# Performance work log

Measured on AMD Instinct MI355X. Metric: run time of the kernel, lower is better.

The kernel has to match this reference:

```python
import jax, jax.numpy as jnp
import numpy as np

D_MODEL = 1024
N_HEADS = 16
HEAD_DIM = D_MODEL // N_HEADS  # 64
WINDOW = 64
HALF = WINDOW // 2  # query i attends keys in [i-HALF, i+HALF]
CHUNK = WINDOW      # chunk size for banded attention; must be >= HALF and divide S
B, S = 4, 4096


def setup_inputs() -> dict:
    key = jax.random.key(0)
    ks = jax.random.split(key, 6)
    s = 0.02
    D = D_MODEL
    return {
        "x":  jax.random.normal(ks[0], (B, S, D), jnp.float32),
        "Wq": jax.random.normal(ks[1], (D, D), jnp.float32) * s,
        "bq": jnp.zeros((D,), jnp.float32),
        "Wk": jax.random.normal(ks[2], (D, D), jnp.float32) * s,
        "bk": jnp.zeros((D,), jnp.float32),
        "Wv": jax.random.normal(ks[3], (D, D), jnp.float32) * s,
        "bv": jnp.zeros((D,), jnp.float32),
        "Wo": jax.random.normal(ks[4], (D, D), jnp.float32) * s,
        "bo": jnp.zeros((D,), jnp.float32),
    }


def reference(x, Wq, bq, Wk, bk, Wv, bv, Wo, bo):
    # Sliding-window attention (seq_len > 128 path of SparseAttention).
    b, s, d = x.shape
    h, hd = N_HEADS, HEAD_DIM
    scale = 1.0 / np.sqrt(hd).astype(np.float32)

    q = (x @ Wq.T + bq).reshape(b, s, h, hd)
    k = (x @ Wk.T + bk).reshape(b, s, h, hd)
    v = (x @ Wv.T + bv).reshape(b, s, h, hd)

    c = CHUNK
    nb = s // c
    qc = q.reshape(b, nb, c, h, hd)

    # Pad one chunk of zeros on each side; each query chunk attends keys in
    # chunks [n-1, n, n+1] (covers the +/-HALF band since HALF <= c).
    pad = jnp.zeros((b, c, h, hd), q.dtype)
    kp = jnp.concatenate([pad, k, pad], axis=1).reshape(b, nb + 2, c, h, hd)
    vp = jnp.concatenate([pad, v, pad], axis=1).reshape(b, nb + 2, c, h, hd)
    k3 = jnp.concatenate([kp[:, :-2], kp[:, 1:-1], kp[:, 2:]], axis=2)  # [b,nb,3c,h,hd]
    v3 = jnp.concatenate([vp[:, :-2], vp[:, 1:-1], vp[:, 2:]], axis=2)

    # scores: [b,h,nb,c,3c]
    scores = jnp.einsum('bnqhd,bnkhd->bhnqk', qc, k3) * scale

    # Banded validity mask. Global query pos = n*c + i ; global key pos = n*c + j - c.
    i = jnp.arange(c)[:, None]          # [c,1]
    j = jnp.arange(3 * c)[None, :]      # [1,3c]
    rel = j - c - i                     # key_pos - query_pos, [c,3c]
    band = (rel >= -HALF) & (rel <= HALF)
    n = jnp.arange(nb)[:, None, None]   # [nb,1,1]
    keypos = n * c + (j - c)[None, :, :]  # [nb,1,3c]
    valid = band[None, :, :] & (keypos >= 0) & (keypos < s)  # [nb,c,3c]

    attn = jax.nn.softmax(jnp.where(valid[None, None], scores, -jnp.inf), axis=-1)
    ctx = jnp.einsum('bhnqk,bnkhd->bnqhd', attn, v3).reshape(b, s, d)
    return ctx @ Wo.T + bo
```

## Files before the change

kernel.cpp:

```cpp
#include <hip/hip_runtime.h>
#include <hip/hip_bf16.h>
#include <cstdint>
#include <cstddef>

#define D_MODEL 1024
#define NHEADS  16
#define HDIM    64
#define HALFW   32
#define BATCH   4
#define SEQ     4096
#define MROWS   (BATCH*SEQ)

typedef __attribute__((ext_vector_type(8))) short        bf16x8;
typedef __attribute__((ext_vector_type(4))) float        f32x4;
typedef __attribute__((ext_vector_type(4))) unsigned int u32x4;

typedef const __attribute__((address_space(1))) void gvoid_t;
typedef __attribute__((address_space(3))) void       lvoid_t;

__device__ __forceinline__ unsigned short f2bf(float f) {
    unsigned int u = __float_as_uint(f);
    u += 0x7fffu + ((u >> 16) & 1u);
    return (unsigned short)(u >> 16);
}

__device__ __forceinline__ int vswz(int row, int bytecol) {
    return (row * 256 + bytecol) ^ (((row ^ (row >> 3)) & 7) << 4);
}

__global__ __launch_bounds__(256)
void cvt_f32_bf16(const float* __restrict__ src, unsigned short* __restrict__ dst, int n8) {
    int i = blockIdx.x * 256 + threadIdx.x;
    if (i >= n8) return;
    float4 a = *(const float4*)(src + (size_t)i * 8);
    float4 b = *(const float4*)(src + (size_t)i * 8 + 4);
    u32x4 o;
    o[0] = (unsigned)f2bf(a.x) | ((unsigned)f2bf(a.y) << 16);
    o[1] = (unsigned)f2bf(a.z) | ((unsigned)f2bf(a.w) << 16);
    o[2] = (unsigned)f2bf(b.x) | ((unsigned)f2bf(b.y) << 16);
    o[3] = (unsigned)f2bf(b.z) | ((unsigned)f2bf(b.w) << 16);
    *(u32x4*)(dst + (size_t)i * 8) = o;
}

__global__ __launch_bounds__(256)
void cvt4_f32_bf16(const float* __restrict__ s0, const float* __restrict__ s1,
                   const float* __restrict__ s2, const float* __restrict__ s3,
                   unsigned short* __restrict__ d0, unsigned short* __restrict__ d1,
                   unsigned short* __restrict__ d2, unsigned short* __restrict__ d3, int n8) {
    int i = blockIdx.x * 256 + threadIdx.x;
    if (i >= n8) return;
    const float* src = blockIdx.y == 0 ? s0 : blockIdx.y == 1 ? s1 : blockIdx.y == 2 ? s2 : s3;
    unsigned short* dst = blockIdx.y == 0 ? d0 : blockIdx.y == 1 ? d1 : blockIdx.y == 2 ? d2 : d3;
    float4 a = *(const float4*)(src + (size_t)i * 8);
    float4 b = *(const float4*)(src + (size_t)i * 8 + 4);
    u32x4 o;
    o[0] = (unsigned)f2bf(a.x) | ((unsigned)f2bf(a.y) << 16);
    o[1] = (unsigned)f2bf(a.z) | ((unsigned)f2bf(a.w) << 16);
    o[2] = (unsigned)f2bf(b.x) | ((unsigned)f2bf(b.y) << 16);
    o[3] = (unsigned)f2bf(b.z) | ((unsigned)f2bf(b.w) << 16);
    *(u32x4*)(dst + (size_t)i * 8) = o;
}

template <int NOUT, int F32OUT>
__global__ __launch_bounds__(256, 2)
void gemm_db(const unsigned short* __restrict__ A,
             const unsigned short* __restrict__ W0,
             const unsigned short* __restrict__ W1,
             const unsigned short* __restrict__ W2,
             const float* __restrict__ b0, const float* __restrict__ b1,
             const float* __restrict__ b2,
             unsigned short* __restrict__ o0, unsigned short* __restrict__ o1,
             unsigned short* __restrict__ o2, float* __restrict__ of32)
{
    constexpr int K  = 1024;
    constexpr int HT = K / 32;
    constexpr int CBG = 8 * NOUT;
    __shared__ unsigned short lds[2 * 12288];

    const int tid  = threadIdx.x;
    const int wave = tid >> 6, lane = tid & 63;
    const int wr = wave >> 1, wc = wave & 1;

    const int bid = blockIdx.x;
    const int g   = (bid & 7) * (8 * CBG) + (bid >> 3);
    const int rb  = g / CBG;
    const int cbg = g % CBG;
    const int which = cbg >> 3;
    const int bm = rb * 256, bn = (cbg & 7) * 128;

    const unsigned short* W = (NOUT == 1 || which == 0) ? W0 : (which == 1 ? W1 : W2);
    const float* bias       = (NOUT == 1 || which == 0) ? b0 : (which == 1 ? b1 : b2);
    unsigned short* obf     = (NOUT == 1 || which == 0) ? o0 : (which == 1 ? o1 : o2);

    f32x4 acc[8][4];
    #pragma unroll
    for (int m = 0; m < 8; ++m)
        #pragma unroll
        for (int n = 0; n < 4; ++n)
            #pragma unroll
            for (int j = 0; j < 4; ++j) acc[m][n][j] = 0.0f;

    char* ldsb = (char*)lds;

    const int ra  = tid >> 2;
    const int ks  = ((tid & 3) - (ra >> 1)) & 3;
    const size_t sA[4] = { (size_t)(bm + ra) * K + ks * 8,
                           (size_t)(bm + ra + 64)  * K + ks * 8,
                           (size_t)(bm + ra + 128) * K + ks * 8,
                           (size_t)(bm + ra + 192) * K + ks * 8 };
    const size_t sB[2] = { (size_t)(bn + ra) * K + ks * 8,
                           (size_t)(bn + ra + 64)  * K + ks * 8 };
    const int ldsW = wave * 1024;

    auto STAGE = [&](int h) {
        const int slot = (h & 1) * 24576;
        const int ke = h * 32;
        #pragma unroll
        for (int i = 0; i < 4; ++i)
            __builtin_amdgcn_global_load_lds((gvoid_t*)(A + sA[i] + ke),
                (lvoid_t*)(ldsb + slot + ldsW + i * 4096), 16, 0, 0);
        #pragma unroll
        for (int i = 0; i < 2; ++i)
            __builtin_amdgcn_global_load_lds((gvoid_t*)(W + sB[i] + ke),
                (lvoid_t*)(ldsb + slot + 16384 + ldsW + i * 4096), 16, 0, 0);
    };

    const int lr = lane & 15;
    const int pp = (((lane >> 4) + (lr >> 1)) & 3) << 4;
    const int abase = (wr * 128 + lr) * 64 + pp;
    const int bbase = 16384 + (wc * 64 + lr) * 64 + pp;

    STAGE(0);
    __syncthreads();

    #pragma unroll 1
    for (int h = 0; h < HT; ++h) {
        const char* sl = ldsb + (h & 1) * 24576;
        if (h + 1 < HT) STAGE(h + 1);
        bf16x8 fa[8], fb[4];
        #pragma unroll
        for (int m = 0; m < 8; ++m) fa[m] = *(const bf16x8*)(sl + abase + m * 1024);
        #pragma unroll
        for (int n = 0; n < 4; ++n) fb[n] = *(const bf16x8*)(sl + bbase + n * 1024);
        #pragma unroll
        for (int m = 0; m < 8; ++m)
            #pragma unroll
            for (int n = 0; n < 4; ++n)
                acc[m][n] = __builtin_amdgcn_mfma_f32_16x16x32_bf16(fa[m], fb[n], acc[m][n], 0, 0, 0);
        __syncthreads();
    }

    float bvv[4];
    #pragma unroll
    for (int n = 0; n < 4; ++n) bvv[n] = bias[bn + wc * 64 + n * 16 + lr];
    #pragma unroll
    for (int m = 0; m < 8; ++m) {
        #pragma unroll
        for (int j = 0; j < 4; ++j) {
            const int row = bm + wr * 128 + m * 16 + (lane >> 4) * 4 + j;
            #pragma unroll
            for (int n = 0; n < 4; ++n) {
                const int col = bn + wc * 64 + n * 16 + lr;
                const float v = acc[m][n][j] + bvv[n];
                if (F32OUT) of32[(size_t)row * 1024 + col] = v;
                else        obf[(size_t)row * 1024 + col]  = f2bf(v);
            }
        }
    }
}

__global__ __launch_bounds__(256)
void attn_band(const unsigned short* __restrict__ Q,
               const unsigned short* __restrict__ Kk,
               const unsigned short* __restrict__ V,
               unsigned short* __restrict__ Ctx)
{
    __shared__ unsigned short Qs[64 * 72];
    __shared__ unsigned short Ks[128 * 72];
    __shared__ unsigned short Vt[64 * 128];
    __shared__ unsigned short Ps[64 * 128];

    const int qt = blockIdx.x, h = blockIdx.y, b = blockIdx.z;
    const int qbase  = qt * 64;
    const int kstart = qbase - HALFW;
    const int tid = threadIdx.x, wave = tid >> 6, lane = tid & 63;

    const size_t base = (size_t)b * SEQ * D_MODEL + (size_t)h * HDIM;
    const unsigned short* Qb = Q  + base;
    const unsigned short* Kb = Kk + base;
    const unsigned short* Vb = V  + base;
    unsigned short*       Cb = Ctx + base;

    for (int c = tid; c < 512; c += 256) {
        const int row = c >> 3, col = (c & 7) * 8;
        *(u32x4*)(Qs + row * 72 + col) =
            *(const u32x4*)(Qb + (size_t)(qbase + row) * D_MODEL + col);
    }
    for (int c = tid; c < 1024; c += 256) {
        const int krow = c >> 3, col = (c & 7) * 8;
        const int kpos = kstart + krow;
        u32x4 kv;
        if (kpos >= 0 && kpos < SEQ) {
            kv = *(const u32x4*)(Kb + (size_t)kpos * D_MODEL + col);
        } else {
            for (int j = 0; j < 4; ++j) kv[j] = 0u;
        }
        *(u32x4*)(Ks + krow * 72 + col) = kv;
    }
    for (int c = tid; c < 512; c += 256) {
        const int p = c >> 3, dch = c & 7;
        const int k0 = kstart + 2 * p, k1 = k0 + 1;
        u32x4 v0, v1;
        if (k0 >= 0 && k0 < SEQ) {
            v0 = *(const u32x4*)(Vb + (size_t)k0 * D_MODEL + dch * 8);
        } else {
            for (int j = 0; j < 4; ++j) v0[j] = 0u;
        }
        if (k1 >= 0 && k1 < SEQ) {
            v1 = *(const u32x4*)(Vb + (size_t)k1 * D_MODEL + dch * 8);
        } else {
            for (int j = 0; j < 4; ++j) v1[j] = 0u;
        }
        #pragma unroll
        for (int j = 0; j < 8; ++j) {
            const int d = dch * 8 + j;
            const unsigned lo = (v0[j >> 1] >> ((j & 1) * 16)) & 0xffffu;
            const unsigned hi = (v1[j >> 1] >> ((j & 1) * 16)) & 0xffffu;
            *(unsigned*)((char*)Vt + vswz(d, 4 * p)) = lo | (hi << 16);
        }
    }
    __syncthreads();

    f32x4 sc[8];
    #pragma unroll
    for (int c = 0; c < 8; ++c)
        #pragma unroll
        for (int j = 0; j < 4; ++j) sc[c][j] = 0.0f;

    bf16x8 aq[2];
    #pragma unroll
    for (int kc = 0; kc < 2; ++kc)
        aq[kc] = *(const bf16x8*)(Qs + (wave * 16 + (lane & 15)) * 72 + kc * 32 + (lane >> 4) * 8);
    #pragma unroll
    for (int c = 0; c < 8; ++c) {
        #pragma unroll
        for (int kc = 0; kc < 2; ++kc) {
            bf16x8 bk_ = *(const bf16x8*)(Ks + (c * 16 + (lane & 15)) * 72 + kc * 32 + (lane >> 4) * 8);
            sc[c] = __builtin_amdgcn_mfma_f32_16x16x32_bf16(aq[kc], bk_, sc[c], 0, 0, 0);
        }
    }

    const int grp = lane >> 4, colk = lane & 15;
    float rowmax[4] = {-1e30f, -1e30f, -1e30f, -1e30f};
    #pragma unroll
    for (int c = 0; c < 8; ++c) {
        const int kpos = kstart + c * 16 + colk;
        #pragma unroll
        for (int j = 0; j < 4; ++j) {
            const int qpos = qbase + wave * 16 + grp * 4 + j;
            const int rel = kpos - qpos;
            const bool valid = (kpos >= 0) && (kpos < SEQ) && (rel >= -HALFW) && (rel <= HALFW);
            const float v = valid ? sc[c][j] * 0.125f : -1e30f;
            sc[c][j] = v;
            rowmax[j] = fmaxf(rowmax[j], v);
        }
    }
    #pragma unroll
    for (int j = 0; j < 4; ++j)
        #pragma unroll
        for (int m = 1; m < 16; m <<= 1)
            rowmax[j] = fmaxf(rowmax[j], __shfl_xor(rowmax[j], m, 64));

    float rowsum[4] = {0.f, 0.f, 0.f, 0.f};
    #pragma unroll
    for (int c = 0; c < 8; ++c)
        #pragma unroll
        for (int j = 0; j < 4; ++j) {
            const float p = __expf(sc[c][j] - rowmax[j]);
            sc[c][j] = p;
            rowsum[j] += p;
        }
    #pragma unroll
    for (int j = 0; j < 4; ++j)
        #pragma unroll
        for (int m = 1; m < 16; m <<= 1)
            rowsum[j] += __shfl_xor(rowsum[j], m, 64);

    #pragma unroll
    for (int c = 0; c < 8; ++c)
        #pragma unroll
        for (int j = 0; j < 4; ++j)
            *(unsigned short*)((char*)Ps + vswz(wave * 16 + grp * 4 + j, (c * 16 + colk) * 2))
                = f2bf(sc[c][j]);
    __syncthreads();

    f32x4 o[4];
    #pragma unroll
    for (int n = 0; n < 4; ++n)
        #pragma unroll
        for (int j = 0; j < 4; ++j) o[n][j] = 0.0f;
    #pragma unroll
    for (int kc = 0; kc < 4; ++kc) {
        bf16x8 pa = *(const bf16x8*)((const char*)Ps +
                        vswz(wave * 16 + (lane & 15), kc * 64 + (lane >> 4) * 16));
        #pragma unroll
        for (int n = 0; n < 4; ++n) {
            bf16x8 bv_ = *(const bf16x8*)((const char*)Vt +
                            vswz(n * 16 + (lane & 15), kc * 64 + (lane >> 4) * 16));
            o[n] = __builtin_amdgcn_mfma_f32_16x16x32_bf16(pa, bv_, o[n], 0, 0, 0);
        }
    }

    float rinv[4];
    #pragma unroll
    for (int j = 0; j < 4; ++j) rinv[j] = 1.0f / rowsum[j];
    #pragma unroll
    for (int n = 0; n < 4; ++n)
        #pragma unroll
        for (int j = 0; j < 4; ++j) {
            const int q = qbase + wave * 16 + grp * 4 + j;
            Cb[(size_t)q * D_MODEL + n * 16 + colk] = f2bf(o[n][j] * rinv[j]);
        }
}

extern "C" void kernel_launch(void* const* d_in, const int* in_sizes, int n_in,
                              void* d_out, int out_size, void* d_ws, size_t ws_size,
                              hipStream_t stream)
{
    (void)in_sizes; (void)n_in; (void)out_size; (void)ws_size;
    const float* x  = (const float*)d_in[0];
    const float* Wq = (const float*)d_in[1];
    const float* bq = (const float*)d_in[2];
    const float* Wk = (const float*)d_in[3];
    const float* bk = (const float*)d_in[4];
    const float* Wv = (const float*)d_in[5];
    const float* bv = (const float*)d_in[6];
    const float* Wo = (const float*)d_in[7];
    const float* bo = (const float*)d_in[8];
    float* out = (float*)d_out;

    char* ws = (char*)d_ws;
    unsigned short* xb  = (unsigned short*)ws;
    unsigned short* wqb = (unsigned short*)(ws + 33554432);
    unsigned short* wkb = wqb + 1048576;
    unsigned short* wvb = wkb + 1048576;
    unsigned short* wob = wvb + 1048576;
    unsigned short* qb  = wob + 1048576;
    unsigned short* kb  = qb + (size_t)MROWS * D_MODEL;
    unsigned short* vb  = kb + (size_t)MROWS * D_MODEL;
    unsigned short* ctxb = xb;

    cvt_f32_bf16<<<dim3(MROWS * D_MODEL / 8 / 256), 256, 0, stream>>>(x, xb, MROWS * D_MODEL / 8);
    cvt4_f32_bf16<<<dim3(D_MODEL * D_MODEL / 8 / 256, 4), 256, 0, stream>>>(
        Wq, Wk, Wv, Wo, wqb, wkb, wvb, wob, D_MODEL * D_MODEL / 8);

    gemm_db<3, 0><<<dim3(1536), 256, 0, stream>>>(
        xb, wqb, wkb, wvb, bq, bk, bv, qb, kb, vb, nullptr);

    attn_band<<<dim3(SEQ / 64, NHEADS, BATCH), 256, 0, stream>>>(qb, kb, vb, ctxb);

    gemm_db<1, 1><<<dim3(512), 256, 0, stream>>>(
        ctxb, wob, wob, wob, bo, bo, bo, nullptr, nullptr, nullptr, out);
}
```

Baseline: 232.5 us.

## Fuse fp32-to-bf16 input conversion into QKV GEMM and read Q/K directly in attention

Removes the separate x conversion kernel. The QKV GEMM now loads fp32 x into registers, packs it to bf16 with v_cvt_pk_bf16_f32 and writes it into LDS itself, overlapped with the MFMA loop. This avoids a full write and re-read of the bf16 copy of x. The attention kernel drops its Q/K LDS staging and one barrier, loading MFMA fragments straight from global memory. In exchange the GEMM reads twice as many bytes of A per tile, needs more registers, and the attention K loads can go out of the sequence range; those reads land in adjacent workspace and their scores are masked.

```diff
diff --git a/kernel.cpp b/kernel.cpp
--- a/kernel.cpp
+++ b/kernel.cpp
@@ -24,22 +24,14 @@
     return (unsigned short)(u >> 16);
 }
 
+__device__ __forceinline__ unsigned cvtpk(float lo, float hi) {
+    unsigned r;
+    asm("v_cvt_pk_bf16_f32 %0, %1, %2" : "=v"(r) : "v"(lo), "v"(hi));
+    return r;
+}
+
 __device__ __forceinline__ int vswz(int row, int bytecol) {
     return (row * 256 + bytecol) ^ (((row ^ (row >> 3)) & 7) << 4);
-}
-
-__global__ __launch_bounds__(256)
-void cvt_f32_bf16(const float* __restrict__ src, unsigned short* __restrict__ dst, int n8) {
-    int i = blockIdx.x * 256 + threadIdx.x;
-    if (i >= n8) return;
-    float4 a = *(const float4*)(src + (size_t)i * 8);
-    float4 b = *(const float4*)(src + (size_t)i * 8 + 4);
-    u32x4 o;
-    o[0] = (unsigned)f2bf(a.x) | ((unsigned)f2bf(a.y) << 16);
-    o[1] = (unsigned)f2bf(a.z) | ((unsigned)f2bf(a.w) << 16);
-    o[2] = (unsigned)f2bf(b.x) | ((unsigned)f2bf(b.y) << 16);
-    o[3] = (unsigned)f2bf(b.z) | ((unsigned)f2bf(b.w) << 16);
-    *(u32x4*)(dst + (size_t)i * 8) = o;
 }
 
 __global__ __launch_bounds__(256)
@@ -61,20 +53,19 @@
     *(u32x4*)(dst + (size_t)i * 8) = o;
 }
 
-template <int NOUT, int F32OUT>
 __global__ __launch_bounds__(256, 2)
-void gemm_db(const unsigned short* __restrict__ A,
-             const unsigned short* __restrict__ W0,
-             const unsigned short* __restrict__ W1,
-             const unsigned short* __restrict__ W2,
-             const float* __restrict__ b0, const float* __restrict__ b1,
-             const float* __restrict__ b2,
-             unsigned short* __restrict__ o0, unsigned short* __restrict__ o1,
-             unsigned short* __restrict__ o2, float* __restrict__ of32)
+void gemm_qkv(const float* __restrict__ X,
+              const unsigned short* __restrict__ W0,
+              const unsigned short* __restrict__ W1,
+              const unsigned short* __restrict__ W2,
+              const float* __restrict__ b0, const float* __restrict__ b1,
+              const float* __restrict__ b2,
+              unsigned short* __restrict__ o0, unsigned short* __restrict__ o1,
+              unsigned short* __restrict__ o2)
 {
     constexpr int K  = 1024;
     constexpr int HT = K / 32;
-    constexpr int CBG = 8 * NOUT;
+    constexpr int CBG = 24;
     __shared__ unsigned short lds[2 * 12288];
 
     const int tid  = threadIdx.x;
@@ -88,9 +79,126 @@
     const int which = cbg >> 3;
     const int bm = rb * 256, bn = (cbg & 7) * 128;
 
-    const unsigned short* W = (NOUT == 1 || which == 0) ? W0 : (which == 1 ? W1 : W2);
-    const float* bias       = (NOUT == 1 || which == 0) ? b0 : (which == 1 ? b1 : b2);
-    unsigned short* obf     = (NOUT == 1 || which == 0) ? o0 : (which == 1 ? o1 : o2);
+    const unsigned short* W = which == 0 ? W0 : (which == 1 ? W1 : W2);
+    const float* bias       = which == 0 ? b0 : (which == 1 ? b1 : b2);
+    unsigned short* obf     = which == 0 ? o0 : (which == 1 ? o1 : o2);
+
+    f32x4 acc[8][4];
+    #pragma unroll
+    for (int m = 0; m < 8; ++m)
+        #pragma unroll
+        for (int n = 0; n < 4; ++n)
+            #pragma unroll
+            for (int j = 0; j < 4; ++j) acc[m][n][j] = 0.0f;
+
+    char* ldsb = (char*)lds;
+
+    const int ra   = tid >> 2;
+    const int posk = tid & 3;
+    const int ks   = (posk - (ra >> 1)) & 3;
+    size_t sAf[4];
+    #pragma unroll
+    for (int i = 0; i < 4; ++i) sAf[i] = (size_t)(bm + ra + 64 * i) * K + ks * 8;
+    const size_t sB[2] = { (size_t)(bn + ra) * K + ks * 8,
+                           (size_t)(bn + ra + 64) * K + ks * 8 };
+    const int ldsW = wave * 1024;
+    const int aWrite = ra * 64 + posk * 16;
+
+    float4 av[8];
+
+    auto LOADA = [&](int h) {
+        const int ke = h * 32;
+        #pragma unroll
+        for (int i = 0; i < 4; ++i) {
+            av[2 * i]     = *(const float4*)(X + sAf[i] + ke);
+            av[2 * i + 1] = *(const float4*)(X + sAf[i] + ke + 4);
+        }
+    };
+    auto STAGE_B = [&](int h) {
+        const int slot = (h & 1) * 24576;
+        const int ke = h * 32;
+        #pragma unroll
+        for (int i = 0; i < 2; ++i)
+            __builtin_amdgcn_global_load_lds((gvoid_t*)(W + sB[i] + ke),
+                (lvoid_t*)(ldsb + slot + 16384 + ldsW + i * 4096), 16, 0, 0);
+    };
+    auto CVTWR = [&](int h) {
+        const int slot = (h & 1) * 24576;
+        #pragma unroll
+        for (int i = 0; i < 4; ++i) {
+            u32x4 o;
+            o[0] = cvtpk(av[2 * i].x,     av[2 * i].y);
+            o[1] = cvtpk(av[2 * i].z,     av[2 * i].w);
+            o[2] = cvtpk(av[2 * i + 1].x, av[2 * i + 1].y);
+            o[3] = cvtpk(av[2 * i + 1].z, av[2 * i + 1].w);
+            *(u32x4*)(ldsb + slot + i * 4096 + aWrite) = o;
+        }
+    };
+
+    const int lr = lane & 15;
+    const int pp = (((lane >> 4) + (lr >> 1)) & 3) << 4;
+    const int abase = (wr * 128 + lr) * 64 + pp;
+    const int bbase = 16384 + (wc * 64 + lr) * 64 + pp;
+
+    LOADA(0); STAGE_B(0); CVTWR(0);
+    __syncthreads();
+
+    #pragma unroll 1
+    for (int h = 0; h < HT; ++h) {
+        const char* sl = ldsb + (h & 1) * 24576;
+        if (h + 1 < HT) { LOADA(h + 1); STAGE_B(h + 1); }
+        bf16x8 fa[8], fb[4];
+        #pragma unroll
+        for (int m = 0; m < 8; ++m) fa[m] = *(const bf16x8*)(sl + abase + m * 1024);
+        #pragma unroll
+        for (int n = 0; n < 4; ++n) fb[n] = *(const bf16x8*)(sl + bbase + n * 1024);
+        #pragma unroll
+        for (int m = 0; m < 8; ++m)
+            #pragma unroll
+            for (int n = 0; n < 4; ++n)
+                acc[m][n] = __builtin_amdgcn_mfma_f32_16x16x32_bf16(fa[m], fb[n], acc[m][n], 0, 0, 0);
+        if (h + 1 < HT) CVTWR(h + 1);
+        __syncthreads();
+    }
+
+    float bvv[4];
+    #pragma unroll
+    for (int n = 0; n < 4; ++n) bvv[n] = bias[bn + wc * 64 + n * 16 + lr];
+    #pragma unroll
+    for (int m = 0; m < 8; ++m) {
+        #pragma unroll
+        for (int j = 0; j < 4; ++j) {
+            const int row = bm + wr * 128 + m * 16 + (lane >> 4) * 4 + j;
+            #pragma unroll
+            for (int n = 0; n < 4; ++n) {
+                const int col = bn + wc * 64 + n * 16 + lr;
+                obf[(size_t)row * 1024 + col] = f2bf(acc[m][n][j] + bvv[n]);
+            }
+        }
+    }
+}
+
+template <int NOUT, int F32OUT>
+__global__ __launch_bounds__(256, 2)
+void gemm_db(const unsigned short* __restrict__ A,
+             const unsigned short* __restrict__ W0,
+             const float* __restrict__ b0,
+             unsigned short* __restrict__ o0, float* __restrict__ of32)
+{
+    constexpr int K  = 1024;
+    constexpr int HT = K / 32;
+    constexpr int CBG = 8 * NOUT;
+    __shared__ unsigned short lds[2 * 12288];
+
+    const int tid  = threadIdx.x;
+    const int wave = tid >> 6, lane = tid & 63;
+    const int wr = wave >> 1, wc = wave & 1;
+
+    const int bid = blockIdx.x;
+    const int g   = (bid & 7) * (8 * CBG) + (bid >> 3);
+    const int rb  = g / CBG;
+    const int cbg = g % CBG;
+    const int bm = rb * 256, bn = (cbg & 7) * 128;
 
     f32x4 acc[8][4];
     #pragma unroll
@@ -121,7 +229,7 @@
                 (lvoid_t*)(ldsb + slot + ldsW + i * 4096), 16, 0, 0);
         #pragma unroll
         for (int i = 0; i < 2; ++i)
-            __builtin_amdgcn_global_load_lds((gvoid_t*)(W + sB[i] + ke),
+            __builtin_amdgcn_global_load_lds((gvoid_t*)(W0 + sB[i] + ke),
                 (lvoid_t*)(ldsb + slot + 16384 + ldsW + i * 4096), 16, 0, 0);
     };
 
@@ -152,7 +260,7 @@
 
     float bvv[4];
     #pragma unroll
-    for (int n = 0; n < 4; ++n) bvv[n] = bias[bn + wc * 64 + n * 16 + lr];
+    for (int n = 0; n < 4; ++n) bvv[n] = b0[bn + wc * 64 + n * 16 + lr];
     #pragma unroll
     for (int m = 0; m < 8; ++m) {
         #pragma unroll
@@ -163,7 +271,7 @@
                 const int col = bn + wc * 64 + n * 16 + lr;
                 const float v = acc[m][n][j] + bvv[n];
                 if (F32OUT) of32[(size_t)row * 1024 + col] = v;
-                else        obf[(size_t)row * 1024 + col]  = f2bf(v);
+                else        o0[(size_t)row * 1024 + col]  = f2bf(v);
             }
         }
     }
@@ -175,8 +283,6 @@
                const unsigned short* __restrict__ V,
                unsigned short* __restrict__ Ctx)
 {
-    __shared__ unsigned short Qs[64 * 72];
-    __shared__ unsigned short Ks[128 * 72];
     __shared__ unsigned short Vt[64 * 128];
     __shared__ unsigned short Ps[64 * 128];
 
@@ -191,22 +297,6 @@
     const unsigned short* Vb = V  + base;
     unsigned short*       Cb = Ctx + base;
 
-    for (int c = tid; c < 512; c += 256) {
-        const int row = c >> 3, col = (c & 7) * 8;
-        *(u32x4*)(Qs + row * 72 + col) =
-            *(const u32x4*)(Qb + (size_t)(qbase + row) * D_MODEL + col);
-    }
-    for (int c = tid; c < 1024; c += 256) {
-        const int krow = c >> 3, col = (c & 7) * 8;
-        const int kpos = kstart + krow;
-        u32x4 kv;
-        if (kpos >= 0 && kpos < SEQ) {
-            kv = *(const u32x4*)(Kb + (size_t)kpos * D_MODEL + col);
-        } else {
-            for (int j = 0; j < 4; ++j) kv[j] = 0u;
-        }
-        *(u32x4*)(Ks + krow * 72 + col) = kv;
-    }
     for (int c = tid; c < 512; c += 256) {
         const int p = c >> 3, dch = c & 7;
         const int k0 = kstart + 2 * p, k1 = k0 + 1;
@@ -237,15 +327,19 @@
         #pragma unroll
         for (int j = 0; j < 4; ++j) sc[c][j] = 0.0f;
 
+    const int fcol = (lane >> 4) * 8;
     bf16x8 aq[2];
     #pragma unroll
     for (int kc = 0; kc < 2; ++kc)
-        aq[kc] = *(const bf16x8*)(Qs + (wave * 16 + (lane & 15)) * 72 + kc * 32 + (lane >> 4) * 8);
+        aq[kc] = *(const bf16x8*)(Qb + (size_t)(qbase + wave * 16 + (lane & 15)) * D_MODEL
+                                     + kc * 32 + fcol);
     #pragma unroll
     for (int c = 0; c < 8; ++c) {
+        const long krow = (long)kstart + c * 16 + (lane & 15);
+        const unsigned short* kp = Kb + krow * (long)D_MODEL + fcol;
         #pragma unroll
         for (int kc = 0; kc < 2; ++kc) {
-            bf16x8 bk_ = *(const bf16x8*)(Ks + (c * 16 + (lane & 15)) * 72 + kc * 32 + (lane >> 4) * 8);
+            bf16x8 bk_ = *(const bf16x8*)(kp + kc * 32);
             sc[c] = __builtin_amdgcn_mfma_f32_16x16x32_bf16(aq[kc], bk_, sc[c], 0, 0, 0);
         }
     }
@@ -292,7 +386,6 @@
         for (int j = 0; j < 4; ++j)
             *(unsigned short*)((char*)Ps + vswz(wave * 16 + grp * 4 + j, (c * 16 + colk) * 2))
                 = f2bf(sc[c][j]);
-    __syncthreads();
 
     f32x4 o[4];
     #pragma unroll
@@ -340,7 +433,7 @@
     float* out = (float*)d_out;
 
     char* ws = (char*)d_ws;
-    unsigned short* xb  = (unsigned short*)ws;
+    unsigned short* ctxb = (unsigned short*)ws;
     unsigned short* wqb = (unsigned short*)(ws + 33554432);
     unsigned short* wkb = wqb + 1048576;
     unsigned short* wvb = wkb + 1048576;
@@ -348,17 +441,15 @@
     unsigned short* qb  = wob + 1048576;
     unsigned short* kb  = qb + (size_t)MROWS * D_MODEL;
     unsigned short* vb  = kb + (size_t)MROWS * D_MODEL;
-    unsigned short* ctxb = xb;
-
-    cvt_f32_bf16<<<dim3(MROWS * D_MODEL / 8 / 256), 256, 0, stream>>>(x, xb, MROWS * D_MODEL / 8);
+
     cvt4_f32_bf16<<<dim3(D_MODEL * D_MODEL / 8 / 256, 4), 256, 0, stream>>>(
         Wq, Wk, Wv, Wo, wqb, wkb, wvb, wob, D_MODEL * D_MODEL / 8);
 
-    gemm_db<3, 0><<<dim3(1536), 256, 0, stream>>>(
-        xb, wqb, wkb, wvb, bq, bk, bv, qb, kb, vb, nullptr);
+    gemm_qkv<<<dim3(1536), 256, 0, stream>>>(
+        x, wqb, wkb, wvb, bq, bk, bv, qb, kb, vb);
 
     attn_band<<<dim3(SEQ / 64, NHEADS, BATCH), 256, 0, stream>>>(qb, kb, vb, ctxb);
 
     gemm_db<1, 1><<<dim3(512), 256, 0, stream>>>(
-        ctxb, wob, wob, wob, bo, bo, bo, nullptr, nullptr, nullptr, out);
-}
+        ctxb, wob, bo, nullptr, out);
+}
```

New measurement: 267.6 us. 1.15x slower.

## Load GEMM weights and attention Q/K straight from global into registers

Applied to the files above, without the earlier changes.

The projection GEMM no longer stages the weight tile in LDS. Each wave loads its B fragments directly from global memory into registers every K-step, which halves the LDS footprint, and the block-to-tile mapping is reordered. The attention kernel drops its Q and K shared-memory staging and reads the MFMA fragments straight from global; the barrier before the P·V stage is removed because each wave reads only its own P rows. The aim is less LDS traffic and fewer barriers, at the cost of exposed global-load latency with no prefetch, and out-of-range K reads at the sequence edges that are then masked.

```diff
diff --git a/kernel.cpp b/kernel.cpp
--- a/kernel.cpp
+++ b/kernel.cpp
@@ -63,7 +63,7 @@
 
 template <int NOUT, int F32OUT>
 __global__ __launch_bounds__(256, 2)
-void gemm_db(const unsigned short* __restrict__ A,
+void gemm_bd(const unsigned short* __restrict__ A,
              const unsigned short* __restrict__ W0,
              const unsigned short* __restrict__ W1,
              const unsigned short* __restrict__ W2,
@@ -75,16 +75,17 @@
     constexpr int K  = 1024;
     constexpr int HT = K / 32;
     constexpr int CBG = 8 * NOUT;
-    __shared__ unsigned short lds[2 * 12288];
+    __shared__ unsigned short lds[2 * 8192];
 
     const int tid  = threadIdx.x;
     const int wave = tid >> 6, lane = tid & 63;
     const int wr = wave >> 1, wc = wave & 1;
 
     const int bid = blockIdx.x;
-    const int g   = (bid & 7) * (8 * CBG) + (bid >> 3);
-    const int rb  = g / CBG;
-    const int cbg = g % CBG;
+    const int x   = bid & 7;
+    const int lw  = bid >> 3;
+    const int cbg = lw >> 3;
+    const int rb  = x * 8 + (lw & 7);
     const int which = cbg >> 3;
     const int bm = rb * 256, bn = (cbg & 7) * 128;
 
@@ -108,40 +109,38 @@
                            (size_t)(bm + ra + 64)  * K + ks * 8,
                            (size_t)(bm + ra + 128) * K + ks * 8,
                            (size_t)(bm + ra + 192) * K + ks * 8 };
-    const size_t sB[2] = { (size_t)(bn + ra) * K + ks * 8,
-                           (size_t)(bn + ra + 64)  * K + ks * 8 };
     const int ldsW = wave * 1024;
 
-    auto STAGE = [&](int h) {
-        const int slot = (h & 1) * 24576;
+    auto STAGE_A = [&](int h) {
+        const int slot = (h & 1) * 16384;
         const int ke = h * 32;
         #pragma unroll
         for (int i = 0; i < 4; ++i)
             __builtin_amdgcn_global_load_lds((gvoid_t*)(A + sA[i] + ke),
                 (lvoid_t*)(ldsb + slot + ldsW + i * 4096), 16, 0, 0);
-        #pragma unroll
-        for (int i = 0; i < 2; ++i)
-            __builtin_amdgcn_global_load_lds((gvoid_t*)(W + sB[i] + ke),
-                (lvoid_t*)(ldsb + slot + 16384 + ldsW + i * 4096), 16, 0, 0);
     };
 
     const int lr = lane & 15;
     const int pp = (((lane >> 4) + (lr >> 1)) & 3) << 4;
     const int abase = (wr * 128 + lr) * 64 + pp;
-    const int bbase = 16384 + (wc * 64 + lr) * 64 + pp;
-
-    STAGE(0);
+    const unsigned short* wrow[4];
+    #pragma unroll
+    for (int n = 0; n < 4; ++n)
+        wrow[n] = W + (size_t)(bn + wc * 64 + n * 16 + lr) * K + (lane >> 4) * 8;
+
+    STAGE_A(0);
     __syncthreads();
 
     #pragma unroll 1
     for (int h = 0; h < HT; ++h) {
-        const char* sl = ldsb + (h & 1) * 24576;
-        if (h + 1 < HT) STAGE(h + 1);
-        bf16x8 fa[8], fb[4];
+        const char* sl = ldsb + (h & 1) * 16384;
+        if (h + 1 < HT) STAGE_A(h + 1);
+        bf16x8 fb[4];
+        #pragma unroll
+        for (int n = 0; n < 4; ++n) fb[n] = *(const bf16x8*)(wrow[n] + h * 32);
+        bf16x8 fa[8];
         #pragma unroll
         for (int m = 0; m < 8; ++m) fa[m] = *(const bf16x8*)(sl + abase + m * 1024);
-        #pragma unroll
-        for (int n = 0; n < 4; ++n) fb[n] = *(const bf16x8*)(sl + bbase + n * 1024);
         #pragma unroll
         for (int m = 0; m < 8; ++m)
             #pragma unroll
@@ -175,8 +174,6 @@
                const unsigned short* __restrict__ V,
                unsigned short* __restrict__ Ctx)
 {
-    __shared__ unsigned short Qs[64 * 72];
-    __shared__ unsigned short Ks[128 * 72];
     __shared__ unsigned short Vt[64 * 128];
     __shared__ unsigned short Ps[64 * 128];
 
@@ -191,22 +188,6 @@
     const unsigned short* Vb = V  + base;
     unsigned short*       Cb = Ctx + base;
 
-    for (int c = tid; c < 512; c += 256) {
-        const int row = c >> 3, col = (c & 7) * 8;
-        *(u32x4*)(Qs + row * 72 + col) =
-            *(const u32x4*)(Qb + (size_t)(qbase + row) * D_MODEL + col);
-    }
-    for (int c = tid; c < 1024; c += 256) {
-        const int krow = c >> 3, col = (c & 7) * 8;
-        const int kpos = kstart + krow;
-        u32x4 kv;
-        if (kpos >= 0 && kpos < SEQ) {
-            kv = *(const u32x4*)(Kb + (size_t)kpos * D_MODEL + col);
-        } else {
-            for (int j = 0; j < 4; ++j) kv[j] = 0u;
-        }
-        *(u32x4*)(Ks + krow * 72 + col) = kv;
-    }
     for (int c = tid; c < 512; c += 256) {
         const int p = c >> 3, dch = c & 7;
         const int k0 = kstart + 2 * p, k1 = k0 + 1;
@@ -237,15 +218,19 @@
         #pragma unroll
         for (int j = 0; j < 4; ++j) sc[c][j] = 0.0f;
 
+    const int fcol = (lane >> 4) * 8;
     bf16x8 aq[2];
     #pragma unroll
     for (int kc = 0; kc < 2; ++kc)
-        aq[kc] = *(const bf16x8*)(Qs + (wave * 16 + (lane & 15)) * 72 + kc * 32 + (lane >> 4) * 8);
+        aq[kc] = *(const bf16x8*)(Qb + (size_t)(qbase + wave * 16 + (lane & 15)) * D_MODEL
+                                     + kc * 32 + fcol);
     #pragma unroll
     for (int c = 0; c < 8; ++c) {
+        const long krow = (long)kstart + c * 16 + (lane & 15);
+        const unsigned short* kp = Kb + krow * (long)D_MODEL + fcol;
         #pragma unroll
         for (int kc = 0; kc < 2; ++kc) {
-            bf16x8 bk_ = *(const bf16x8*)(Ks + (c * 16 + (lane & 15)) * 72 + kc * 32 + (lane >> 4) * 8);
+            bf16x8 bk_ = *(const bf16x8*)(kp + kc * 32);
             sc[c] = __builtin_amdgcn_mfma_f32_16x16x32_bf16(aq[kc], bk_, sc[c], 0, 0, 0);
         }
     }
@@ -292,7 +277,6 @@
         for (int j = 0; j < 4; ++j)
             *(unsigned short*)((char*)Ps + vswz(wave * 16 + grp * 4 + j, (c * 16 + colk) * 2))
                 = f2bf(sc[c][j]);
-    __syncthreads();
 
     f32x4 o[4];
     #pragma unroll
@@ -354,11 +338,11 @@
     cvt4_f32_bf16<<<dim3(D_MODEL * D_MODEL / 8 / 256, 4), 256, 0, stream>>>(
         Wq, Wk, Wv, Wo, wqb, wkb, wvb, wob, D_MODEL * D_MODEL / 8);
 
-    gemm_db<3, 0><<<dim3(1536), 256, 0, stream>>>(
+    gemm_bd<3, 0><<<dim3(1536), 256, 0, stream>>>(
         xb, wqb, wkb, wvb, bq, bk, bv, qb, kb, vb, nullptr);
 
     attn_band<<<dim3(SEQ / 64, NHEADS, BATCH), 256, 0, stream>>>(qb, kb, vb, ctxb);
 
-    gemm_db<1, 1><<<dim3(512), 256, 0, stream>>>(
+    gemm_bd<1, 1><<<dim3(512), 256, 0, stream>>>(
         ctxb, wob, wob, wob, bo, bo, bo, nullptr, nullptr, nullptr, out);
 }
```

Result: slower. 277.0 us (+19.1%).
